# Kernel tuning notes

Hardware: AMD Instinct MI355X
Metric: run time of the kernel (lower is better)

The kernel has to match this reference:

```python
import jax, jax.numpy as jnp
import numpy as np

MODES = 16
WIDTH = 64
DEPTH = 4
MLP = 128


def spectral_conv(x, w_cplx):
    # x: [B, C, H, W] float32; w_cplx: [C, C, m1, m2] complex64
    B, C, H, W = x.shape
    x_ft = jnp.fft.rfft2(x)  # [B, C, H, W//2+1] complex
    m1, m2 = MODES, MODES
    low = jnp.einsum('bixy,ioxy->boxy', x_ft[:, :, :m1, :m2], w_cplx)
    out_ft = jnp.zeros((B, C, H, W // 2 + 1), dtype=jnp.complex64)
    out_ft = out_ft.at[:, :, :m1, :m2].set(low)
    return jnp.fft.irfft2(out_ft, s=(H, W)).astype(x.dtype)


def conv1x1(x, w, b):
    # x: [B,Cin,H,W], w: [Cout,Cin], b: [Cout]
    return jnp.einsum('bihw,oi->bohw', x, w) + b[None, :, None, None]


def setup_inputs() -> dict:
    key = jax.random.key(0)
    ks = jax.random.split(key, 4 + 4 * DEPTH)
    inp = {}
    inp['x'] = jax.random.normal(ks[0], (8, 3, 256, 256), dtype=jnp.float32)
    inp['fc0_w'] = jax.random.normal(ks[1], (WIDTH, 3), dtype=jnp.float32) * 0.1
    inp['fc0_b'] = jnp.zeros((WIDTH,), dtype=jnp.float32)
    scale = 1.0 / (WIDTH * WIDTH)
    sw_re, sw_im, ww, wb = [], [], [], []
    for i in range(DEPTH):
        k1, k2, k3 = jax.random.split(ks[4 + i], 3)
        sw_re.append(scale * jax.random.uniform(k1, (WIDTH, WIDTH, MODES, MODES), dtype=jnp.float32))
        sw_im.append(scale * jax.random.uniform(k2, (WIDTH, WIDTH, MODES, MODES), dtype=jnp.float32))
        ww.append(jax.random.normal(k3, (WIDTH, WIDTH), dtype=jnp.float32) * 0.05)
        wb.append(jnp.zeros((WIDTH,), dtype=jnp.float32))
    inp['spec_w_re'] = jnp.stack(sw_re)  # [D, C, C, m1, m2]
    inp['spec_w_im'] = jnp.stack(sw_im)
    inp['w_w'] = jnp.stack(ww)           # [D, C, C]
    inp['w_b'] = jnp.stack(wb)           # [D, C]
    inp['fc1_w'] = jax.random.normal(ks[2], (MLP, WIDTH), dtype=jnp.float32) * 0.05
    inp['fc1_b'] = jnp.zeros((MLP,), dtype=jnp.float32)
    inp['fc2_w'] = jax.random.normal(ks[3], (3, MLP), dtype=jnp.float32) * 0.05
    inp['fc2_b'] = jnp.zeros((3,), dtype=jnp.float32)
    return inp


def reference(x, fc0_w, fc0_b, spec_w_re, spec_w_im, w_w, w_b, fc1_w, fc1_b, fc2_w, fc2_b):
    # Dropout is identity in eval mode.
    h = conv1x1(x, fc0_w, fc0_b)  # [B, WIDTH, H, W]
    for i in range(DEPTH):
        w_cplx = spec_w_re[i] + 1j * spec_w_im[i]
        x1 = spectral_conv(h, w_cplx)
        x2 = conv1x1(h, w_w[i], w_b[i])
        h = jax.nn.relu(x1 + x2)
    h = jnp.transpose(h, (0, 2, 3, 1))  # [B, H, W, WIDTH]
    h = jax.nn.relu(jnp.einsum('bhwc,mc->bhwm', h, fc1_w) + fc1_b)
    h = jnp.einsum('bhwm,om->bhwo', h, fc2_w) + fc2_b
    return jnp.transpose(h, (0, 3, 1, 2))  # [B, 3, H, W]
```

## Files before the change

kernel.cpp:

```cpp
#include <hip/hip_runtime.h>

#define Hd 256
#define Wd 256
#define HW 65536
#define C 64
#define B 8
#define M 16
#define NDEPTH 4
#define NMLP 128

typedef __attribute__((ext_vector_type(8))) __bf16 bf16x8;
typedef __attribute__((ext_vector_type(4))) float f32x4;

__device__ inline void split_pack8(const float* v, uint4& hq, uint4& lq) {
    unsigned hw[4], lw[4];
#pragma unroll
    for (int i = 0; i < 4; ++i) {
        float a = v[2 * i], bb = v[2 * i + 1];
        unsigned ua = __float_as_uint(a);
        unsigned ha = (ua + 0x7fffu + ((ua >> 16) & 1u)) & 0xffff0000u;
        float ra = a - __uint_as_float(ha);
        unsigned ural = __float_as_uint(ra);
        unsigned la = (ural + 0x7fffu + ((ural >> 16) & 1u)) >> 16;
        unsigned ub = __float_as_uint(bb);
        unsigned hb = (ub + 0x7fffu + ((ub >> 16) & 1u)) & 0xffff0000u;
        float rb = bb - __uint_as_float(hb);
        unsigned urbl = __float_as_uint(rb);
        unsigned lb = (urbl + 0x7fffu + ((urbl >> 16) & 1u)) >> 16;
        hw[i] = (ha >> 16) | (hb & 0xffff0000u);
        lw[i] = la | (lb << 16);
    }
    hq = make_uint4(hw[0], hw[1], hw[2], hw[3]);
    lq = make_uint4(lw[0], lw[1], lw[2], lw[3]);
}

__global__ void k_table(float2* __restrict__ tab) {
    int t = threadIdx.x;
    double a = (6.283185307179586476925286766559 / 256.0) * (double)t;
    tab[t] = make_float2((float)cos(a), (float)sin(a));
}

__global__ void k_prep0(const float2* __restrict__ tab, const float* __restrict__ fc1w,
                        const float* __restrict__ ww,
                        float* __restrict__ trig, float* __restrict__ trigFT,
                        float* __restrict__ w1T, float* __restrict__ wwT_all) {
    int blk = blockIdx.x, t = threadIdx.x;
    if (blk < 32) {
        int k = blk & 15;
        float2 e = tab[(k * t) & 255];
        trig[blk * 256 + t] = (blk < 16) ? e.x : e.y;
    } else if (blk < 64) {
        int f = (blk - 32) * 256 + t;
        int y = f >> 5, kk = f & 31;
        float2 e = tab[((kk & 15) * y) & 255];
        trigFT[f] = (kk < 16) ? e.x : -e.y;
    } else if (blk < 96) {
        int f = (blk - 64) * 256 + t;
        int i = f >> 7, m = f & 127;
        w1T[f] = fc1w[m * 64 + i];
    } else {
        int f = (blk - 96) * 256 + t;
        int d = f >> 12, r = f & 4095;
        int i = r >> 6, o = r & 63;
        wwT_all[f] = ww[d * 4096 + o * 64 + i];
    }
}

__global__ void k_prep_et(const float2* __restrict__ tab,
                          uint4* __restrict__ ETh, uint4* __restrict__ ETl) {
    int c = blockIdx.x * 256 + threadIdx.x;
    if (c >= 1024) return;
    int ph = c >> 7, kc = (c >> 5) & 3, m = c & 31;
    float v[8];
#pragma unroll
    for (int j = 0; j < 8; ++j) {
        int y = ph * 32 + kc * 8 + j;
        float2 e = tab[((m & 15) * y) & 255];
        v[j] = (m < 16) ? e.x : -e.y;
    }
    uint4 hq, lq;
    split_pack8(v, hq, lq);
    ETh[c] = hq; ETl[c] = lq;
}

__global__ void k_fc0(const float* __restrict__ x, const float* __restrict__ w,
                      const float* __restrict__ bias, float* __restrict__ h) {
    int p = blockIdx.x * 256 + threadIdx.x;
    int b = p >> 16, pix = p & 65535;
    float x0 = x[(b * 3 + 0) * HW + pix];
    float x1 = x[(b * 3 + 1) * HW + pix];
    float x2 = x[(b * 3 + 2) * HW + pix];
    for (int o = 0; o < C; ++o) {
        float v = bias[o];
        v = fmaf(w[o * 3 + 0], x0, v);
        v = fmaf(w[o * 3 + 1], x1, v);
        v = fmaf(w[o * 3 + 2], x2, v);
        h[(b * C + o) * HW + pix] = v;
    }
}

__global__ __launch_bounds__(256, 4)
void k_fwd_y(const float* __restrict__ h, const uint4* __restrict__ ETh,
             const uint4* __restrict__ ETl, float* __restrict__ T1F) {
    __shared__ uint4 sBh[512], sBl[512];
    int blk = blockIdx.x;
    int xh = blk & 1, bc = blk >> 1;
    int x0 = xh * 128;
    int t = threadIdx.x;
    int xs = t & 127, half = t >> 7;
    int w = t >> 6, l = t & 63;
    int lr = l & 15, lq = l >> 4;
    f32x4 acc[2][2];
#pragma unroll
    for (int u = 0; u < 2; ++u)
#pragma unroll
        for (int xt = 0; xt < 2; ++xt) {
            acc[u][xt][0] = 0.f; acc[u][xt][1] = 0.f;
            acc[u][xt][2] = 0.f; acc[u][xt][3] = 0.f;
        }
    for (int ph = 0; ph < 8; ++ph) {
        {
            const float* src = h + (size_t)bc * HW + (ph * 32 + half * 16) * 256 + x0 + xs;
            float v[16];
#pragma unroll
            for (int kk = 0; kk < 16; ++kk) v[kk] = src[kk * 256];
#pragma unroll
            for (int c2 = 0; c2 < 2; ++c2) {
                uint4 hq4, lq4;
                split_pack8(v + c2 * 8, hq4, lq4);
                int cell = (half * 2 + c2) * 128 + xs;
                sBh[cell] = hq4; sBl[cell] = lq4;
            }
        }
        __syncthreads();
        bf16x8 Ah[2], Al[2];
#pragma unroll
        for (int u = 0; u < 2; ++u) {
            int ci = ph * 128 + lq * 32 + u * 16 + lr;
            Ah[u] = __builtin_bit_cast(bf16x8, ETh[ci]);
            Al[u] = __builtin_bit_cast(bf16x8, ETl[ci]);
        }
#pragma unroll
        for (int xt = 0; xt < 2; ++xt) {
            bf16x8 Bh = __builtin_bit_cast(bf16x8, sBh[lq * 128 + w * 32 + xt * 16 + lr]);
            bf16x8 Bl = __builtin_bit_cast(bf16x8, sBl[lq * 128 + w * 32 + xt * 16 + lr]);
#pragma unroll
            for (int u = 0; u < 2; ++u) {
                acc[u][xt] = __builtin_amdgcn_mfma_f32_16x16x32_bf16(Ah[u], Bh, acc[u][xt], 0, 0, 0);
                acc[u][xt] = __builtin_amdgcn_mfma_f32_16x16x32_bf16(Ah[u], Bl, acc[u][xt], 0, 0, 0);
                acc[u][xt] = __builtin_amdgcn_mfma_f32_16x16x32_bf16(Al[u], Bh, acc[u][xt], 0, 0, 0);
            }
        }
        __syncthreads();
    }
#pragma unroll
    for (int u = 0; u < 2; ++u)
#pragma unroll
        for (int xt = 0; xt < 2; ++xt)
#pragma unroll
            for (int g = 0; g < 4; ++g)
                T1F[(size_t)bc * 8192 + (u * 16 + lq * 4 + g) * 256 + x0 + w * 32 + xt * 16 + lr] =
                    acc[u][xt][g];
}

__global__ __launch_bounds__(256, 2)
void k_fwd_x(const float* __restrict__ T1F, const float* __restrict__ trig,
             float2* __restrict__ X) {
    __shared__ float sT[32 * 260];
    __shared__ float sG[32 * 260];
    int bc = blockIdx.x, t = threadIdx.x;
#pragma unroll
    for (int p = 0; p < 8; ++p) {
        int f = t + p * 256;
        int row = f >> 6, seg = f & 63;
        ((float4*)(sT + row * 260))[seg] = *(const float4*)(T1F + (size_t)bc * 8192 + f * 4);
        ((float4*)(sG + row * 260))[seg] = *(const float4*)(trig + row * 256 + seg * 4);
    }
    __syncthreads();
    int ky = t >> 4, kx = t & 15;
    const float* Tr = sT + ky * 260;
    const float* Ti = sT + (16 + ky) * 260;
    const float* Cs = sG + kx * 260;
    const float* Sn = sG + (16 + kx) * 260;
    float xr0 = 0.f, xi0 = 0.f, xr1 = 0.f, xi1 = 0.f;
    for (int q = 0; q < 64; q += 2) {
        float4 tr = *(const float4*)(Tr + q * 4);
        float4 ti = *(const float4*)(Ti + q * 4);
        float4 cs = *(const float4*)(Cs + q * 4);
        float4 sn = *(const float4*)(Sn + q * 4);
        xr0 = fmaf(tr.x, cs.x, xr0); xr0 = fmaf(ti.x, sn.x, xr0);
        xi0 = fmaf(ti.x, cs.x, xi0); xi0 = fmaf(-tr.x, sn.x, xi0);
        xr0 = fmaf(tr.y, cs.y, xr0); xr0 = fmaf(ti.y, sn.y, xr0);
        xi0 = fmaf(ti.y, cs.y, xi0); xi0 = fmaf(-tr.y, sn.y, xi0);
        xr0 = fmaf(tr.z, cs.z, xr0); xr0 = fmaf(ti.z, sn.z, xr0);
        xi0 = fmaf(ti.z, cs.z, xi0); xi0 = fmaf(-tr.z, sn.z, xi0);
        xr0 = fmaf(tr.w, cs.w, xr0); xr0 = fmaf(ti.w, sn.w, xr0);
        xi0 = fmaf(ti.w, cs.w, xi0); xi0 = fmaf(-tr.w, sn.w, xi0);
        float4 tr1 = *(const float4*)(Tr + q * 4 + 4);
        float4 ti1 = *(const float4*)(Ti + q * 4 + 4);
        float4 cs1 = *(const float4*)(Cs + q * 4 + 4);
        float4 sn1 = *(const float4*)(Sn + q * 4 + 4);
        xr1 = fmaf(tr1.x, cs1.x, xr1); xr1 = fmaf(ti1.x, sn1.x, xr1);
        xi1 = fmaf(ti1.x, cs1.x, xi1); xi1 = fmaf(-tr1.x, sn1.x, xi1);
        xr1 = fmaf(tr1.y, cs1.y, xr1); xr1 = fmaf(ti1.y, sn1.y, xr1);
        xi1 = fmaf(ti1.y, cs1.y, xi1); xi1 = fmaf(-tr1.y, sn1.y, xi1);
        xr1 = fmaf(tr1.z, cs1.z, xr1); xr1 = fmaf(ti1.z, sn1.z, xr1);
        xi1 = fmaf(ti1.z, cs1.z, xi1); xi1 = fmaf(-tr1.z, sn1.z, xi1);
        xr1 = fmaf(tr1.w, cs1.w, xr1); xr1 = fmaf(ti1.w, sn1.w, xr1);
        xi1 = fmaf(ti1.w, cs1.w, xi1); xi1 = fmaf(-tr1.w, sn1.w, xi1);
    }
    X[bc * 256 + t] = make_float2(xr0 + xr1, xi0 + xi1);
}

__global__ __launch_bounds__(256, 2)
void k_mix(const float2* __restrict__ X, const float* __restrict__ wre,
           const float* __restrict__ wim, float2* __restrict__ Y) {
    int o = blockIdx.x >> 2;
    int bq = blockIdx.x & 3;
    int m = threadIdx.x;
    int b0 = bq * 2, b1 = bq * 2 + 1;
    float yr0 = 0.f, yi0 = 0.f, yr1 = 0.f, yi1 = 0.f;
    for (int i = 0; i < C; ++i) {
        float wr = wre[(i * C + o) * 256 + m];
        float wi = wim[(i * C + o) * 256 + m];
        float2 x0 = X[(b0 * C + i) * 256 + m];
        float2 x1 = X[(b1 * C + i) * 256 + m];
        yr0 = fmaf(x0.x, wr, fmaf(-x0.y, wi, yr0));
        yi0 = fmaf(x0.x, wi, fmaf(x0.y, wr, yi0));
        yr1 = fmaf(x1.x, wr, fmaf(-x1.y, wi, yr1));
        yi1 = fmaf(x1.x, wi, fmaf(x1.y, wr, yi1));
    }
    Y[(b0 * C + o) * 256 + m] = make_float2(yr0, yi0);
    Y[(b1 * C + o) * 256 + m] = make_float2(yr1, yi1);
}

__global__ __launch_bounds__(256, 2)
void k_invy(const float2* __restrict__ Y, const float2* __restrict__ tab,
            float* __restrict__ Gq) {
    __shared__ float2 st[256];
    int blk = blockIdx.x;
    int yt = blk & 15, pg = (blk >> 4) & 3, b = blk >> 6;
    int t = threadIdx.x;
    st[t] = tab[t];
    int o = t & 63, kx = pg * 4 + (t >> 6);
    __syncthreads();
    float sc = (kx == 0 ? 1.0f : 2.0f) * (1.0f / 65536.0f);
    float yr[16], yi[16];
    const float2* yp = Y + (size_t)(b * 64 + o) * 256 + kx;
#pragma unroll
    for (int ky = 0; ky < 16; ++ky) {
        float2 v = yp[ky * 16];
        yr[ky] = v.x * sc;
        yi[ky] = v.y * sc;
    }
    int y0 = yt * 16;
    for (int yy = 0; yy < 16; ++yy) {
        int y = y0 + yy;
        float re = 0.f, im = 0.f;
#pragma unroll
        for (int ky = 0; ky < 16; ++ky) {
            float2 e = st[(ky * y) & 255];
            re = fmaf(yr[ky], e.x, re);
            re = fmaf(-yi[ky], e.y, re);
            im = fmaf(yr[ky], e.y, im);
            im = fmaf(yi[ky], e.x, im);
        }
        float* gp = Gq + (size_t)(b * 256 + y) * 32 * 64 + o;
        gp[kx * 64] = re;
        gp[(16 + kx) * 64] = -im;
    }
}

__global__ __launch_bounds__(256, 4)
void k_final(float* __restrict__ h, const float* __restrict__ Gq,
             const float* __restrict__ wwT, const float* __restrict__ wb,
             const float* __restrict__ trig) {
    __shared__ uint4 sHh[512], sHl[512];
    __shared__ uint4 sWh[256], sWl[256];
    int blk = blockIdx.x;
    int xq = blk & 1, y = (blk >> 1) & 255, b = blk >> 9;
    int x0 = xq * 128;
    int t = threadIdx.x;
    int xs = t & 127, half = t >> 7;
    int os = t & 63, q = t >> 6;
    int w = t >> 6, l = t & 63;
    int lr = l & 15, lq = l >> 4;
    f32x4 acc[8];
    {
        int ob = w * 16 + lq * 4;
        f32x4 ini;
        ini[0] = wb[ob]; ini[1] = wb[ob + 1]; ini[2] = wb[ob + 2]; ini[3] = wb[ob + 3];
#pragma unroll
        for (int xt = 0; xt < 8; ++xt) acc[xt] = ini;
    }
    for (int ph = 0; ph < 3; ++ph) {
        {
            const float* src; size_t str;
            if (ph < 2) {
                src = h + (size_t)(b * 64 + ph * 32 + half * 16) * HW + y * 256 + x0 + xs;
                str = HW;
            } else {
                src = trig + (half * 16) * 256 + x0 + xs;
                str = 256;
            }
            float v[16];
#pragma unroll
            for (int kk = 0; kk < 16; ++kk) v[kk] = src[(size_t)kk * str];
#pragma unroll
            for (int c2 = 0; c2 < 2; ++c2) {
                uint4 hq4, lq4;
                split_pack8(v + c2 * 8, hq4, lq4);
                int cell = (half * 2 + c2) * 128 + xs;
                sHh[cell] = hq4; sHl[cell] = lq4;
            }
        }
        {
            const float* src = (ph < 2)
                ? (wwT + (ph * 32 + q * 8) * 64 + os)
                : (Gq + ((size_t)(b * 256 + y) * 32 + q * 8) * 64 + os);
            float v[8];
#pragma unroll
            for (int kk = 0; kk < 8; ++kk) v[kk] = src[kk * 64];
            uint4 hq4, lq4;
            split_pack8(v, hq4, lq4);
            int cell = q * 64 + os;
            sWh[cell] = hq4; sWl[cell] = lq4;
        }
        __syncthreads();
        bf16x8 Ah = __builtin_bit_cast(bf16x8, sWh[lq * 64 + w * 16 + lr]);
        bf16x8 Al = __builtin_bit_cast(bf16x8, sWl[lq * 64 + w * 16 + lr]);
#pragma unroll
        for (int xt = 0; xt < 8; ++xt) {
            bf16x8 Bh = __builtin_bit_cast(bf16x8, sHh[lq * 128 + xt * 16 + lr]);
            bf16x8 Bl = __builtin_bit_cast(bf16x8, sHl[lq * 128 + xt * 16 + lr]);
            acc[xt] = __builtin_amdgcn_mfma_f32_16x16x32_bf16(Ah, Bh, acc[xt], 0, 0, 0);
            acc[xt] = __builtin_amdgcn_mfma_f32_16x16x32_bf16(Ah, Bl, acc[xt], 0, 0, 0);
            acc[xt] = __builtin_amdgcn_mfma_f32_16x16x32_bf16(Al, Bh, acc[xt], 0, 0, 0);
        }
        __syncthreads();
    }
#pragma unroll
    for (int g = 0; g < 4; ++g) {
        int o = w * 16 + lq * 4 + g;
        float* dst = h + (size_t)(b * 64 + o) * HW + y * 256 + x0 + lr;
#pragma unroll
        for (int xt = 0; xt < 8; ++xt)
            dst[xt * 16] = fmaxf(acc[xt][g], 0.f);
    }
}

__global__ __launch_bounds__(256, 3)
void k_fc12(const float* __restrict__ h, const float* __restrict__ w1T,
            const float* __restrict__ b1, const float* __restrict__ w2,
            const float* __restrict__ b2, float* __restrict__ out) {
    __shared__ uint4 sHh[512], sHl[512];
    __shared__ uint4 sWh[512], sWl[512];
    int blk = blockIdx.x;
    int xq = blk & 1, y = (blk >> 1) & 255, b = blk >> 9;
    int x0 = xq * 128;
    int t = threadIdx.x;
    int xs = t & 127, half = t >> 7;
    int w = t >> 6, l = t & 63;
    int lr = l & 15, lq = l >> 4;
    int mb = w * 32;
    f32x4 acc[2][8];
#pragma unroll
    for (int u = 0; u < 2; ++u) {
        int m0 = mb + u * 16 + lq * 4;
        f32x4 ini;
        ini[0] = b1[m0]; ini[1] = b1[m0 + 1]; ini[2] = b1[m0 + 2]; ini[3] = b1[m0 + 3];
#pragma unroll
        for (int xt = 0; xt < 8; ++xt) acc[u][xt] = ini;
    }
    for (int ph = 0; ph < 2; ++ph) {
        {
            const float* src = h + (size_t)(b * 64 + ph * 32 + half * 16) * HW + y * 256 + x0 + xs;
            float v[16];
#pragma unroll
            for (int kk = 0; kk < 16; ++kk) v[kk] = src[(size_t)kk * HW];
#pragma unroll
            for (int c2 = 0; c2 < 2; ++c2) {
                uint4 hq4, lq4;
                split_pack8(v + c2 * 8, hq4, lq4);
                int cell = (half * 2 + c2) * 128 + xs;
                sHh[cell] = hq4; sHl[cell] = lq4;
            }
        }
        {
            const float* src = w1T + (ph * 32 + half * 16) * 128 + xs;
            float v[16];
#pragma unroll
            for (int kk = 0; kk < 16; ++kk) v[kk] = src[kk * 128];
#pragma unroll
            for (int c2 = 0; c2 < 2; ++c2) {
                uint4 hq4, lq4;
                split_pack8(v + c2 * 8, hq4, lq4);
                int cell = (half * 2 + c2) * 128 + xs;
                sWh[cell] = hq4; sWl[cell] = lq4;
            }
        }
        __syncthreads();
        bf16x8 Ah[2], Al[2];
#pragma unroll
        for (int u = 0; u < 2; ++u) {
            Ah[u] = __builtin_bit_cast(bf16x8, sWh[lq * 128 + mb + u * 16 + lr]);
            Al[u] = __builtin_bit_cast(bf16x8, sWl[lq * 128 + mb + u * 16 + lr]);
        }
#pragma unroll
        for (int xt = 0; xt < 8; ++xt) {
            bf16x8 Bh = __builtin_bit_cast(bf16x8, sHh[lq * 128 + xt * 16 + lr]);
            bf16x8 Bl = __builtin_bit_cast(bf16x8, sHl[lq * 128 + xt * 16 + lr]);
#pragma unroll
            for (int u = 0; u < 2; ++u) {
                acc[u][xt] = __builtin_amdgcn_mfma_f32_16x16x32_bf16(Ah[u], Bh, acc[u][xt], 0, 0, 0);
                acc[u][xt] = __builtin_amdgcn_mfma_f32_16x16x32_bf16(Ah[u], Bl, acc[u][xt], 0, 0, 0);
                acc[u][xt] = __builtin_amdgcn_mfma_f32_16x16x32_bf16(Al[u], Bh, acc[u][xt], 0, 0, 0);
            }
        }
        __syncthreads();
    }
    float pj[3][8];
#pragma unroll
    for (int j = 0; j < 3; ++j)
#pragma unroll
        for (int xt = 0; xt < 8; ++xt) pj[j][xt] = 0.f;
#pragma unroll
    for (int u = 0; u < 2; ++u)
#pragma unroll
        for (int g = 0; g < 4; ++g) {
            int m = mb + u * 16 + lq * 4 + g;
            float w20 = w2[m], w21 = w2[NMLP + m], w22 = w2[2 * NMLP + m];
#pragma unroll
            for (int xt = 0; xt < 8; ++xt) {
                float r = fmaxf(acc[u][xt][g], 0.f);
                pj[0][xt] = fmaf(w20, r, pj[0][xt]);
                pj[1][xt] = fmaf(w21, r, pj[1][xt]);
                pj[2][xt] = fmaf(w22, r, pj[2][xt]);
            }
        }
#pragma unroll
    for (int j = 0; j < 3; ++j)
#pragma unroll
        for (int xt = 0; xt < 8; ++xt) {
            float v = pj[j][xt];
            v += __shfl_xor(v, 16);
            v += __shfl_xor(v, 32);
            pj[j][xt] = v;
        }
    float* part = (float*)sHh;
    if (lq == 0) {
#pragma unroll
        for (int j = 0; j < 3; ++j)
#pragma unroll
            for (int xt = 0; xt < 8; ++xt)
                part[(w * 3 + j) * 128 + xt * 16 + lr] = pj[j][xt];
    }
    __syncthreads();
#pragma unroll
    for (int r = 0; r < 2; ++r) {
        int idx = t + r * 256;
        if (idx < 384) {
            int j = idx >> 7, xx = idx & 127;
            float s = b2[j];
#pragma unroll
            for (int ww2 = 0; ww2 < 4; ++ww2) s += part[(ww2 * 3 + j) * 128 + xx];
            out[(size_t)(b * 3 + j) * HW + y * 256 + x0 + xx] = s;
        }
    }
}

extern "C" void kernel_launch(void* const* d_in, const int* in_sizes, int n_in,
                              void* d_out, int out_size, void* d_ws, size_t ws_size,
                              hipStream_t stream) {
    const float* x     = (const float*)d_in[0];
    const float* fc0_w = (const float*)d_in[1];
    const float* fc0_b = (const float*)d_in[2];
    const float* swre  = (const float*)d_in[3];
    const float* swim  = (const float*)d_in[4];
    const float* ww    = (const float*)d_in[5];
    const float* wb    = (const float*)d_in[6];
    const float* fc1w  = (const float*)d_in[7];
    const float* fc1b  = (const float*)d_in[8];
    const float* fc2w  = (const float*)d_in[9];
    const float* fc2b  = (const float*)d_in[10];

    float* ws = (float*)d_ws;
    float2* tab    = (float2*)ws;
    float*  h      = ws + 512;
    float*  T1F    = ws + 33554944;
    float2* X      = (float2*)(ws + 37749248);
    float2* Y      = (float2*)(ws + 38011392);
    float*  Gq     = ws + 38273536;
    float*  wwT    = ws + 42467840;
    float*  w1T    = ws + 42484224;
    float*  trig   = ws + 42492416;
    float*  trigFT = ws + 42500608;
    uint4*  ETh    = (uint4*)(ws + 42508800);
    uint4*  ETl    = (uint4*)(ws + 42512896);

    k_table<<<dim3(1), dim3(256), 0, stream>>>(tab);
    k_prep0<<<dim3(160), dim3(256), 0, stream>>>(tab, fc1w, ww, trig, trigFT, w1T, wwT);
    k_prep_et<<<dim3(4), dim3(256), 0, stream>>>(tab, ETh, ETl);
    k_fc0<<<dim3(2048), dim3(256), 0, stream>>>(x, fc0_w, fc0_b, h);

    for (int d = 0; d < NDEPTH; ++d) {
        k_fwd_y<<<dim3(1024), dim3(256), 0, stream>>>(h, ETh, ETl, T1F);
        k_fwd_x<<<dim3(512), dim3(256), 0, stream>>>(T1F, trig, X);
        k_mix<<<dim3(256), dim3(256), 0, stream>>>(X, swre + (size_t)d * C * C * 256,
                                                   swim + (size_t)d * C * C * 256, Y);
        k_invy<<<dim3(512), dim3(256), 0, stream>>>(Y, tab, Gq);
        k_final<<<dim3(4096), dim3(256), 0, stream>>>(h, Gq, wwT + d * 4096, wb + d * C, trig);
    }
    k_fc12<<<dim3(4096), dim3(256), 0, stream>>>(h, w1T, fc1b, fc2w, fc2b, (float*)d_out);
}
```

Before: 630.5 us.

## Register double-buffer global loads and use lgkm-only barriers in GEMM kernels

```diff
diff --git a/kernel.cpp b/kernel.cpp
--- a/kernel.cpp
+++ b/kernel.cpp
@@ -11,6 +11,11 @@
 
 typedef __attribute__((ext_vector_type(8))) __bf16 bf16x8;
 typedef __attribute__((ext_vector_type(4))) float f32x4;
+
+__device__ inline void bar_lgkm() {
+    asm volatile("s_waitcnt lgkmcnt(0)" ::: "memory");
+    __builtin_amdgcn_s_barrier();
+}
 
 __device__ inline void split_pack8(const float* v, uint4& hq, uint4& lq) {
     unsigned hw[4], lw[4];
@@ -118,21 +123,30 @@
             acc[u][xt][0] = 0.f; acc[u][xt][1] = 0.f;
             acc[u][xt][2] = 0.f; acc[u][xt][3] = 0.f;
         }
+    const float* hb = h + (size_t)bc * HW + (half * 16) * 256 + x0 + xs;
+    float v0[16], v1[16];
+    auto loadv = [&](float* vv, int ph) {
+        const float* src = hb + ph * 32 * 256;
+#pragma unroll
+        for (int kk = 0; kk < 16; ++kk) vv[kk] = src[kk * 256];
+    };
+    auto stage = [&](const float* vv) {
+#pragma unroll
+        for (int c2 = 0; c2 < 2; ++c2) {
+            uint4 hq4, lq4;
+            split_pack8(vv + c2 * 8, hq4, lq4);
+            int cell = (half * 2 + c2) * 128 + xs;
+            sBh[cell] = hq4; sBl[cell] = lq4;
+        }
+    };
+    loadv(v0, 0);
+#pragma unroll
     for (int ph = 0; ph < 8; ++ph) {
-        {
-            const float* src = h + (size_t)bc * HW + (ph * 32 + half * 16) * 256 + x0 + xs;
-            float v[16];
-#pragma unroll
-            for (int kk = 0; kk < 16; ++kk) v[kk] = src[kk * 256];
-#pragma unroll
-            for (int c2 = 0; c2 < 2; ++c2) {
-                uint4 hq4, lq4;
-                split_pack8(v + c2 * 8, hq4, lq4);
-                int cell = (half * 2 + c2) * 128 + xs;
-                sBh[cell] = hq4; sBl[cell] = lq4;
-            }
-        }
-        __syncthreads();
+        const float* cur = (ph & 1) ? v1 : v0;
+        float* nxt = (ph & 1) ? v0 : v1;
+        if (ph < 7) loadv(nxt, ph + 1);
+        stage(cur);
+        bar_lgkm();
         bf16x8 Ah[2], Al[2];
 #pragma unroll
         for (int u = 0; u < 2; ++u) {
@@ -151,7 +165,7 @@
                 acc[u][xt] = __builtin_amdgcn_mfma_f32_16x16x32_bf16(Al[u], Bh, acc[u][xt], 0, 0, 0);
             }
         }
-        __syncthreads();
+        bar_lgkm();
     }
 #pragma unroll
     for (int u = 0; u < 2; ++u)
@@ -293,40 +307,48 @@
 #pragma unroll
         for (int xt = 0; xt < 8; ++xt) acc[xt] = ini;
     }
+    float vh0[16], vh1[16], vw0[8], vw1[8];
+    auto loadH = [&](float* vv, int ph) {
+        const float* src; size_t str;
+        if (ph < 2) {
+            src = h + (size_t)(b * 64 + ph * 32 + half * 16) * HW + y * 256 + x0 + xs;
+            str = HW;
+        } else {
+            src = trig + (half * 16) * 256 + x0 + xs;
+            str = 256;
+        }
+#pragma unroll
+        for (int kk = 0; kk < 16; ++kk) vv[kk] = src[(size_t)kk * str];
+    };
+    auto loadW = [&](float* vv, int ph) {
+        const float* src = (ph < 2)
+            ? (wwT + (ph * 32 + q * 8) * 64 + os)
+            : (Gq + ((size_t)(b * 256 + y) * 32 + q * 8) * 64 + os);
+#pragma unroll
+        for (int kk = 0; kk < 8; ++kk) vv[kk] = src[kk * 64];
+    };
+    loadH(vh0, 0); loadW(vw0, 0);
+#pragma unroll
     for (int ph = 0; ph < 3; ++ph) {
+        const float* cH = (ph & 1) ? vh1 : vh0;
+        float* nH = (ph & 1) ? vh0 : vh1;
+        const float* cW = (ph & 1) ? vw1 : vw0;
+        float* nW = (ph & 1) ? vw0 : vw1;
+        if (ph < 2) { loadH(nH, ph + 1); loadW(nW, ph + 1); }
+#pragma unroll
+        for (int c2 = 0; c2 < 2; ++c2) {
+            uint4 hq4, lq4;
+            split_pack8(cH + c2 * 8, hq4, lq4);
+            int cell = (half * 2 + c2) * 128 + xs;
+            sHh[cell] = hq4; sHl[cell] = lq4;
+        }
         {
-            const float* src; size_t str;
-            if (ph < 2) {
-                src = h + (size_t)(b * 64 + ph * 32 + half * 16) * HW + y * 256 + x0 + xs;
-                str = HW;
-            } else {
-                src = trig + (half * 16) * 256 + x0 + xs;
-                str = 256;
-            }
-            float v[16];
-#pragma unroll
-            for (int kk = 0; kk < 16; ++kk) v[kk] = src[(size_t)kk * str];
-#pragma unroll
-            for (int c2 = 0; c2 < 2; ++c2) {
-                uint4 hq4, lq4;
-                split_pack8(v + c2 * 8, hq4, lq4);
-                int cell = (half * 2 + c2) * 128 + xs;
-                sHh[cell] = hq4; sHl[cell] = lq4;
-            }
-        }
-        {
-            const float* src = (ph < 2)
-                ? (wwT + (ph * 32 + q * 8) * 64 + os)
-                : (Gq + ((size_t)(b * 256 + y) * 32 + q * 8) * 64 + os);
-            float v[8];
-#pragma unroll
-            for (int kk = 0; kk < 8; ++kk) v[kk] = src[kk * 64];
             uint4 hq4, lq4;
-            split_pack8(v, hq4, lq4);
+            split_pack8(cW, hq4, lq4);
             int cell = q * 64 + os;
             sWh[cell] = hq4; sWl[cell] = lq4;
         }
-        __syncthreads();
+        bar_lgkm();
         bf16x8 Ah = __builtin_bit_cast(bf16x8, sWh[lq * 64 + w * 16 + lr]);
         bf16x8 Al = __builtin_bit_cast(bf16x8, sWl[lq * 64 + w * 16 + lr]);
 #pragma unroll
@@ -337,7 +359,7 @@
             acc[xt] = __builtin_amdgcn_mfma_f32_16x16x32_bf16(Ah, Bl, acc[xt], 0, 0, 0);
             acc[xt] = __builtin_amdgcn_mfma_f32_16x16x32_bf16(Al, Bh, acc[xt], 0, 0, 0);
         }
-        __syncthreads();
+        bar_lgkm();
     }
 #pragma unroll
     for (int g = 0; g < 4; ++g) {
@@ -349,7 +371,7 @@
     }
 }
 
-__global__ __launch_bounds__(256, 3)
+__global__ __launch_bounds__(256, 4)
 void k_fc12(const float* __restrict__ h, const float* __restrict__ w1T,
             const float* __restrict__ b1, const float* __restrict__ w2,
             const float* __restrict__ b2, float* __restrict__ out) {
@@ -372,19 +394,24 @@
 #pragma unroll
         for (int xt = 0; xt < 8; ++xt) acc[u][xt] = ini;
     }
+    float vh0[16], vh1[16];
+    auto loadH = [&](float* vv, int ph) {
+        const float* src = h + (size_t)(b * 64 + ph * 32 + half * 16) * HW + y * 256 + x0 + xs;
+#pragma unroll
+        for (int kk = 0; kk < 16; ++kk) vv[kk] = src[(size_t)kk * HW];
+    };
+    loadH(vh0, 0);
+#pragma unroll
     for (int ph = 0; ph < 2; ++ph) {
-        {
-            const float* src = h + (size_t)(b * 64 + ph * 32 + half * 16) * HW + y * 256 + x0 + xs;
-            float v[16];
-#pragma unroll
-            for (int kk = 0; kk < 16; ++kk) v[kk] = src[(size_t)kk * HW];
-#pragma unroll
-            for (int c2 = 0; c2 < 2; ++c2) {
-                uint4 hq4, lq4;
-                split_pack8(v + c2 * 8, hq4, lq4);
-                int cell = (half * 2 + c2) * 128 + xs;
-                sHh[cell] = hq4; sHl[cell] = lq4;
-            }
+        const float* cH = (ph & 1) ? vh1 : vh0;
+        float* nH = (ph & 1) ? vh0 : vh1;
+        if (ph < 1) loadH(nH, ph + 1);
+#pragma unroll
+        for (int c2 = 0; c2 < 2; ++c2) {
+            uint4 hq4, lq4;
+            split_pack8(cH + c2 * 8, hq4, lq4);
+            int cell = (half * 2 + c2) * 128 + xs;
+            sHh[cell] = hq4; sHl[cell] = lq4;
         }
         {
             const float* src = w1T + (ph * 32 + half * 16) * 128 + xs;
@@ -399,7 +426,7 @@
                 sWh[cell] = hq4; sWl[cell] = lq4;
             }
         }
-        __syncthreads();
+        bar_lgkm();
         bf16x8 Ah[2], Al[2];
 #pragma unroll
         for (int u = 0; u < 2; ++u) {
@@ -417,7 +444,7 @@
                 acc[u][xt] = __builtin_amdgcn_mfma_f32_16x16x32_bf16(Al[u], Bh, acc[u][xt], 0, 0, 0);
             }
         }
-        __syncthreads();
+        bar_lgkm();
     }
     float pj[3][8];
 #pragma unroll
```

Measured after the change: 618.5 us. Within noise of the previous version (-1.9%).

## Store activations as pre-split bf16 hi/lo in MFMA-ready channel-packed layout

Applied to the files above, without the earlier changes.

```diff
diff --git a/kernel.cpp b/kernel.cpp
--- a/kernel.cpp
+++ b/kernel.cpp
@@ -11,6 +11,11 @@
 
 typedef __attribute__((ext_vector_type(8))) __bf16 bf16x8;
 typedef __attribute__((ext_vector_type(4))) float f32x4;
+
+__device__ inline void bar_lgkm() {
+    asm volatile("s_waitcnt lgkmcnt(0)" ::: "memory");
+    __builtin_amdgcn_s_barrier();
+}
 
 __device__ inline void split_pack8(const float* v, uint4& hq, uint4& lq) {
     unsigned hw[4], lw[4];
@@ -34,6 +39,29 @@
     lq = make_uint4(lw[0], lw[1], lw[2], lw[3]);
 }
 
+__device__ inline void split_pack4(const float* v, uint2& hq, uint2& lq) {
+    unsigned hw[2], lw[2];
+#pragma unroll
+    for (int i = 0; i < 2; ++i) {
+        float a = v[2 * i], bb = v[2 * i + 1];
+        unsigned ua = __float_as_uint(a);
+        unsigned ha = (ua + 0x7fffu + ((ua >> 16) & 1u)) & 0xffff0000u;
+        float ra = a - __uint_as_float(ha);
+        unsigned ural = __float_as_uint(ra);
+        unsigned la = (ural + 0x7fffu + ((ural >> 16) & 1u)) >> 16;
+        unsigned ub = __float_as_uint(bb);
+        unsigned hb = (ub + 0x7fffu + ((ub >> 16) & 1u)) & 0xffff0000u;
+        float rb = bb - __uint_as_float(hb);
+        unsigned urbl = __float_as_uint(rb);
+        unsigned lb = (urbl + 0x7fffu + ((urbl >> 16) & 1u)) >> 16;
+        hw[i] = (ha >> 16) | (hb & 0xffff0000u);
+        lw[i] = la | (lb << 16);
+    }
+    hq = make_uint2(hw[0], hw[1]);
+    lq = make_uint2(lw[0], lw[1]);
+}
+
+
 __global__ void k_table(float2* __restrict__ tab) {
     int t = threadIdx.x;
     double a = (6.283185307179586476925286766559 / 256.0) * (double)t;
@@ -41,28 +69,45 @@
 }
 
 __global__ void k_prep0(const float2* __restrict__ tab, const float* __restrict__ fc1w,
-                        const float* __restrict__ ww,
-                        float* __restrict__ trig, float* __restrict__ trigFT,
-                        float* __restrict__ w1T, float* __restrict__ wwT_all) {
+                        const float* __restrict__ ww, float* __restrict__ trig,
+                        uint4* __restrict__ trigs_h, uint4* __restrict__ trigs_l,
+                        uint4* __restrict__ wws_h, uint4* __restrict__ wws_l,
+                        uint4* __restrict__ w1s_h, uint4* __restrict__ w1s_l) {
     int blk = blockIdx.x, t = threadIdx.x;
     if (blk < 32) {
         int k = blk & 15;
         float2 e = tab[(k * t) & 255];
         trig[blk * 256 + t] = (blk < 16) ? e.x : e.y;
-    } else if (blk < 64) {
-        int f = (blk - 32) * 256 + t;
-        int y = f >> 5, kk = f & 31;
-        float2 e = tab[((kk & 15) * y) & 255];
-        trigFT[f] = (kk < 16) ? e.x : -e.y;
-    } else if (blk < 96) {
-        int f = (blk - 64) * 256 + t;
-        int i = f >> 7, m = f & 127;
-        w1T[f] = fc1w[m * 64 + i];
+    } else if (blk < 36) {
+        int idx = (blk - 32) * 256 + t;
+        int kc = idx >> 8, x = idx & 255;
+        float v[8];
+#pragma unroll
+        for (int j = 0; j < 8; ++j) {
+            int row = kc * 8 + j;
+            float2 e = tab[((row & 15) * x) & 255];
+            v[j] = (row < 16) ? e.x : e.y;
+        }
+        uint4 hq, lq; split_pack8(v, hq, lq);
+        trigs_h[idx] = hq; trigs_l[idx] = lq;
+    } else if (blk < 44) {
+        int idx = (blk - 36) * 256 + t;
+        int o = idx & 63, kc = (idx >> 6) & 3, ph = (idx >> 8) & 1, d = idx >> 9;
+        float v[8];
+#pragma unroll
+        for (int j = 0; j < 8; ++j)
+            v[j] = ww[d * 4096 + o * 64 + ph * 32 + kc * 8 + j];
+        uint4 hq, lq; split_pack8(v, hq, lq);
+        wws_h[idx] = hq; wws_l[idx] = lq;
     } else {
-        int f = (blk - 96) * 256 + t;
-        int d = f >> 12, r = f & 4095;
-        int i = r >> 6, o = r & 63;
-        wwT_all[f] = ww[d * 4096 + o * 64 + i];
+        int idx = (blk - 44) * 256 + t;
+        int m = idx & 127, kc = (idx >> 7) & 3, ph = idx >> 9;
+        float v[8];
+#pragma unroll
+        for (int j = 0; j < 8; ++j)
+            v[j] = fc1w[m * 64 + ph * 32 + kc * 8 + j];
+        uint4 hq, lq; split_pack8(v, hq, lq);
+        w1s_h[idx] = hq; w1s_l[idx] = lq;
     }
 }
 
@@ -84,27 +129,43 @@
 }
 
 __global__ void k_fc0(const float* __restrict__ x, const float* __restrict__ w,
-                      const float* __restrict__ bias, float* __restrict__ h) {
+                      const float* __restrict__ bias,
+                      uint4* __restrict__ hs_h, uint4* __restrict__ hs_l) {
     int p = blockIdx.x * 256 + threadIdx.x;
     int b = p >> 16, pix = p & 65535;
+    int y = pix >> 8, xx = pix & 255;
     float x0 = x[(b * 3 + 0) * HW + pix];
     float x1 = x[(b * 3 + 1) * HW + pix];
     float x2 = x[(b * 3 + 2) * HW + pix];
-    for (int o = 0; o < C; ++o) {
-        float v = bias[o];
-        v = fmaf(w[o * 3 + 0], x0, v);
-        v = fmaf(w[o * 3 + 1], x1, v);
-        v = fmaf(w[o * 3 + 2], x2, v);
-        h[(b * C + o) * HW + pix] = v;
+    size_t rb = (size_t)(b * 256 + y) * 8;
+#pragma unroll
+    for (int cc = 0; cc < 8; ++cc) {
+        float v[8];
+#pragma unroll
+        for (int j = 0; j < 8; ++j) {
+            int o = cc * 8 + j;
+            float s = bias[o];
+            s = fmaf(w[o * 3 + 0], x0, s);
+            s = fmaf(w[o * 3 + 1], x1, s);
+            s = fmaf(w[o * 3 + 2], x2, s);
+            v[j] = s;
+        }
+        uint4 hq, lq; split_pack8(v, hq, lq);
+        size_t cell = (rb + cc) * 256 + xx;
+        hs_h[cell] = hq; hs_l[cell] = lq;
     }
 }
 
 __global__ __launch_bounds__(256, 4)
-void k_fwd_y(const float* __restrict__ h, const uint4* __restrict__ ETh,
-             const uint4* __restrict__ ETl, float* __restrict__ T1F) {
+void k_fwd_y(const uint4* __restrict__ hs_h, const uint4* __restrict__ hs_l,
+             const uint4* __restrict__ ETh, const uint4* __restrict__ ETl,
+             float* __restrict__ T1F) {
     __shared__ uint4 sBh[512], sBl[512];
     int blk = blockIdx.x;
-    int xh = blk & 1, bc = blk >> 1;
+    int rest = blk & 127, cl = blk >> 7;
+    int cc = rest & 7, xh = (rest >> 3) & 1, b = rest >> 4;
+    int c = cc * 8 + cl;
+    int bc = b * 64 + c;
     int x0 = xh * 128;
     int t = threadIdx.x;
     int xs = t & 127, half = t >> 7;
@@ -118,21 +179,45 @@
             acc[u][xt][0] = 0.f; acc[u][xt][1] = 0.f;
             acc[u][xt][2] = 0.f; acc[u][xt][3] = 0.f;
         }
+    const ushort* ph16 = (const ushort*)hs_h;
+    const ushort* pl16 = (const ushort*)hs_l;
+    size_t cbase = ((size_t)(b * 256) * 8 + cc) * 256 + x0 + xs;
+    unsigned hv0[16], lv0[16], hv1[16], lv1[16];
+    auto loadv = [&](unsigned* hv, unsigned* lv, int ph) {
+        size_t a = (cbase + (size_t)(ph * 32 + half * 16) * 2048) * 8 + cl;
+#pragma unroll
+        for (int kk = 0; kk < 16; ++kk) {
+            hv[kk] = ph16[a + kk * 16384];
+            lv[kk] = pl16[a + kk * 16384];
+        }
+    };
+    auto stage = [&](const unsigned* hv, const unsigned* lv) {
+#pragma unroll
+        for (int c2 = 0; c2 < 2; ++c2) {
+            int o8 = c2 * 8;
+            uint4 hq, lqq;
+            hq.x = hv[o8 + 0] | (hv[o8 + 1] << 16);
+            hq.y = hv[o8 + 2] | (hv[o8 + 3] << 16);
+            hq.z = hv[o8 + 4] | (hv[o8 + 5] << 16);
+            hq.w = hv[o8 + 6] | (hv[o8 + 7] << 16);
+            lqq.x = lv[o8 + 0] | (lv[o8 + 1] << 16);
+            lqq.y = lv[o8 + 2] | (lv[o8 + 3] << 16);
+            lqq.z = lv[o8 + 4] | (lv[o8 + 5] << 16);
+            lqq.w = lv[o8 + 6] | (lv[o8 + 7] << 16);
+            int cell = (half * 2 + c2) * 128 + xs;
+            sBh[cell] = hq; sBl[cell] = lqq;
+        }
+    };
+    loadv(hv0, lv0, 0);
+#pragma unroll
     for (int ph = 0; ph < 8; ++ph) {
-        {
-            const float* src = h + (size_t)bc * HW + (ph * 32 + half * 16) * 256 + x0 + xs;
-            float v[16];
-#pragma unroll
-            for (int kk = 0; kk < 16; ++kk) v[kk] = src[kk * 256];
-#pragma unroll
-            for (int c2 = 0; c2 < 2; ++c2) {
-                uint4 hq4, lq4;
-                split_pack8(v + c2 * 8, hq4, lq4);
-                int cell = (half * 2 + c2) * 128 + xs;
-                sBh[cell] = hq4; sBl[cell] = lq4;
-            }
-        }
-        __syncthreads();
+        const unsigned* chv = (ph & 1) ? hv1 : hv0;
+        const unsigned* clv = (ph & 1) ? lv1 : lv0;
+        unsigned* nhv = (ph & 1) ? hv0 : hv1;
+        unsigned* nlv = (ph & 1) ? lv0 : lv1;
+        if (ph < 7) loadv(nhv, nlv, ph + 1);
+        stage(chv, clv);
+        bar_lgkm();
         bf16x8 Ah[2], Al[2];
 #pragma unroll
         for (int u = 0; u < 2; ++u) {
@@ -151,7 +236,7 @@
                 acc[u][xt] = __builtin_amdgcn_mfma_f32_16x16x32_bf16(Al[u], Bh, acc[u][xt], 0, 0, 0);
             }
         }
-        __syncthreads();
+        bar_lgkm();
     }
 #pragma unroll
     for (int u = 0; u < 2; ++u)
@@ -272,19 +357,22 @@
 }
 
 __global__ __launch_bounds__(256, 4)
-void k_final(float* __restrict__ h, const float* __restrict__ Gq,
-             const float* __restrict__ wwT, const float* __restrict__ wb,
-             const float* __restrict__ trig) {
-    __shared__ uint4 sHh[512], sHl[512];
-    __shared__ uint4 sWh[256], sWl[256];
+void k_final(uint4* __restrict__ hs_h, uint4* __restrict__ hs_l,
+             const float* __restrict__ Gq,
+             const uint4* __restrict__ wws_h, const uint4* __restrict__ wws_l,
+             const float* __restrict__ wb,
+             const uint4* __restrict__ trigs_h, const uint4* __restrict__ trigs_l) {
+    __shared__ uint4 sH0h[512], sH0l[512], sH1h[512], sH1l[512];
+    __shared__ uint4 sGh[256], sGl[256];
     int blk = blockIdx.x;
     int xq = blk & 1, y = (blk >> 1) & 255, b = blk >> 9;
     int x0 = xq * 128;
     int t = threadIdx.x;
-    int xs = t & 127, half = t >> 7;
     int os = t & 63, q = t >> 6;
     int w = t >> 6, l = t & 63;
     int lr = l & 15, lq = l >> 4;
+    int kc0 = t >> 7, xsa = t & 127;
+    size_t hbase = (size_t)(b * 256 + y) * 8;
     f32x4 acc[8];
     {
         int ob = w * 16 + lq * 4;
@@ -293,76 +381,97 @@
 #pragma unroll
         for (int xt = 0; xt < 8; ++xt) acc[xt] = ini;
     }
-    for (int ph = 0; ph < 3; ++ph) {
-        {
-            const float* src; size_t str;
-            if (ph < 2) {
-                src = h + (size_t)(b * 64 + ph * 32 + half * 16) * HW + y * 256 + x0 + xs;
-                str = HW;
-            } else {
-                src = trig + (half * 16) * 256 + x0 + xs;
-                str = 256;
-            }
-            float v[16];
-#pragma unroll
-            for (int kk = 0; kk < 16; ++kk) v[kk] = src[(size_t)kk * str];
-#pragma unroll
-            for (int c2 = 0; c2 < 2; ++c2) {
-                uint4 hq4, lq4;
-                split_pack8(v + c2 * 8, hq4, lq4);
-                int cell = (half * 2 + c2) * 128 + xs;
-                sHh[cell] = hq4; sHl[cell] = lq4;
-            }
-        }
-        {
-            const float* src = (ph < 2)
-                ? (wwT + (ph * 32 + q * 8) * 64 + os)
-                : (Gq + ((size_t)(b * 256 + y) * 32 + q * 8) * 64 + os);
-            float v[8];
-#pragma unroll
-            for (int kk = 0; kk < 8; ++kk) v[kk] = src[kk * 64];
-            uint4 hq4, lq4;
-            split_pack8(v, hq4, lq4);
-            int cell = q * 64 + os;
-            sWh[cell] = hq4; sWl[cell] = lq4;
-        }
-        __syncthreads();
-        bf16x8 Ah = __builtin_bit_cast(bf16x8, sWh[lq * 64 + w * 16 + lr]);
-        bf16x8 Al = __builtin_bit_cast(bf16x8, sWl[lq * 64 + w * 16 + lr]);
+    float gv[8];
+    {
+        const float* gsrc = Gq + ((size_t)(b * 256 + y) * 32 + q * 8) * 64 + os;
+#pragma unroll
+        for (int kk = 0; kk < 8; ++kk) gv[kk] = gsrc[kk * 64];
+    }
+    uint4 A0h = wws_h[lq * 64 + w * 16 + lr];
+    uint4 A0l = wws_l[lq * 64 + w * 16 + lr];
+    uint4 A1h = wws_h[(4 + lq) * 64 + w * 16 + lr];
+    uint4 A1l = wws_l[(4 + lq) * 64 + w * 16 + lr];
+    uint4 h0a = hs_h[(hbase + kc0) * 256 + x0 + xsa];
+    uint4 l0a = hs_l[(hbase + kc0) * 256 + x0 + xsa];
+    uint4 h0b = hs_h[(hbase + 2 + kc0) * 256 + x0 + xsa];
+    uint4 l0b = hs_l[(hbase + 2 + kc0) * 256 + x0 + xsa];
+    uint4 h1a = hs_h[(hbase + 4 + kc0) * 256 + x0 + xsa];
+    uint4 l1a = hs_l[(hbase + 4 + kc0) * 256 + x0 + xsa];
+    uint4 h1b = hs_h[(hbase + 6 + kc0) * 256 + x0 + xsa];
+    uint4 l1b = hs_l[(hbase + 6 + kc0) * 256 + x0 + xsa];
+    {
+        uint4 ghq, glq; split_pack8(gv, ghq, glq);
+        sGh[q * 64 + os] = ghq; sGl[q * 64 + os] = glq;
+    }
+    sH0h[t] = h0a; sH0h[t + 256] = h0b;
+    sH0l[t] = l0a; sH0l[t + 256] = l0b;
+    bar_lgkm();
+    sH1h[t] = h1a; sH1h[t + 256] = h1b;
+    sH1l[t] = l1a; sH1l[t + 256] = l1b;
+#pragma unroll
+    for (int xt = 0; xt < 8; ++xt) {
+        bf16x8 Bh = __builtin_bit_cast(bf16x8, sH0h[lq * 128 + xt * 16 + lr]);
+        bf16x8 Bl = __builtin_bit_cast(bf16x8, sH0l[lq * 128 + xt * 16 + lr]);
+        bf16x8 Ah = __builtin_bit_cast(bf16x8, A0h);
+        bf16x8 Al = __builtin_bit_cast(bf16x8, A0l);
+        acc[xt] = __builtin_amdgcn_mfma_f32_16x16x32_bf16(Ah, Bh, acc[xt], 0, 0, 0);
+        acc[xt] = __builtin_amdgcn_mfma_f32_16x16x32_bf16(Ah, Bl, acc[xt], 0, 0, 0);
+        acc[xt] = __builtin_amdgcn_mfma_f32_16x16x32_bf16(Al, Bh, acc[xt], 0, 0, 0);
+    }
+    bar_lgkm();
+#pragma unroll
+    for (int xt = 0; xt < 8; ++xt) {
+        bf16x8 Bh = __builtin_bit_cast(bf16x8, sH1h[lq * 128 + xt * 16 + lr]);
+        bf16x8 Bl = __builtin_bit_cast(bf16x8, sH1l[lq * 128 + xt * 16 + lr]);
+        bf16x8 Ah = __builtin_bit_cast(bf16x8, A1h);
+        bf16x8 Al = __builtin_bit_cast(bf16x8, A1l);
+        acc[xt] = __builtin_amdgcn_mfma_f32_16x16x32_bf16(Ah, Bh, acc[xt], 0, 0, 0);
+        acc[xt] = __builtin_amdgcn_mfma_f32_16x16x32_bf16(Ah, Bl, acc[xt], 0, 0, 0);
+        acc[xt] = __builtin_amdgcn_mfma_f32_16x16x32_bf16(Al, Bh, acc[xt], 0, 0, 0);
+    }
+    {
+        bf16x8 Ah = __builtin_bit_cast(bf16x8, sGh[lq * 64 + w * 16 + lr]);
+        bf16x8 Al = __builtin_bit_cast(bf16x8, sGl[lq * 64 + w * 16 + lr]);
 #pragma unroll
         for (int xt = 0; xt < 8; ++xt) {
-            bf16x8 Bh = __builtin_bit_cast(bf16x8, sHh[lq * 128 + xt * 16 + lr]);
-            bf16x8 Bl = __builtin_bit_cast(bf16x8, sHl[lq * 128 + xt * 16 + lr]);
+            bf16x8 Bh = __builtin_bit_cast(bf16x8, trigs_h[lq * 256 + x0 + xt * 16 + lr]);
+            bf16x8 Bl = __builtin_bit_cast(bf16x8, trigs_l[lq * 256 + x0 + xt * 16 + lr]);
             acc[xt] = __builtin_amdgcn_mfma_f32_16x16x32_bf16(Ah, Bh, acc[xt], 0, 0, 0);
             acc[xt] = __builtin_amdgcn_mfma_f32_16x16x32_bf16(Ah, Bl, acc[xt], 0, 0, 0);
             acc[xt] = __builtin_amdgcn_mfma_f32_16x16x32_bf16(Al, Bh, acc[xt], 0, 0, 0);
         }
-        __syncthreads();
-    }
-#pragma unroll
-    for (int g = 0; g < 4; ++g) {
-        int o = w * 16 + lq * 4 + g;
-        float* dst = h + (size_t)(b * 64 + o) * HW + y * 256 + x0 + lr;
-#pragma unroll
-        for (int xt = 0; xt < 8; ++xt)
-            dst[xt * 16] = fmaxf(acc[xt][g], 0.f);
+    }
+    uint2* hp_h = (uint2*)hs_h;
+    uint2* hp_l = (uint2*)hs_l;
+    int ccw = w * 2 + (lq >> 1);
+    int halfsel = lq & 1;
+#pragma unroll
+    for (int xt = 0; xt < 8; ++xt) {
+        float r[4];
+#pragma unroll
+        for (int g = 0; g < 4; ++g) r[g] = fmaxf(acc[xt][g], 0.f);
+        uint2 hq, lqd; split_pack4(r, hq, lqd);
+        size_t gc = (hbase + ccw) * 256 + x0 + xt * 16 + lr;
+        hp_h[gc * 2 + halfsel] = hq;
+        hp_l[gc * 2 + halfsel] = lqd;
     }
 }
 
 __global__ __launch_bounds__(256, 3)
-void k_fc12(const float* __restrict__ h, const float* __restrict__ w1T,
+void k_fc12(const uint4* __restrict__ hs_h, const uint4* __restrict__ hs_l,
+            const uint4* __restrict__ w1s_h, const uint4* __restrict__ w1s_l,
             const float* __restrict__ b1, const float* __restrict__ w2,
             const float* __restrict__ b2, float* __restrict__ out) {
-    __shared__ uint4 sHh[512], sHl[512];
-    __shared__ uint4 sWh[512], sWl[512];
+    __shared__ uint4 sH0h[512], sH0l[512], sH1h[512], sH1l[512];
     int blk = blockIdx.x;
     int xq = blk & 1, y = (blk >> 1) & 255, b = blk >> 9;
     int x0 = xq * 128;
     int t = threadIdx.x;
-    int xs = t & 127, half = t >> 7;
     int w = t >> 6, l = t & 63;
     int lr = l & 15, lq = l >> 4;
     int mb = w * 32;
+    int kc0 = t >> 7, xsa = t & 127;
+    size_t hbase = (size_t)(b * 256 + y) * 8;
     f32x4 acc[2][8];
 #pragma unroll
     for (int u = 0; u < 2; ++u) {
@@ -372,52 +481,53 @@
 #pragma unroll
         for (int xt = 0; xt < 8; ++xt) acc[u][xt] = ini;
     }
-    for (int ph = 0; ph < 2; ++ph) {
-        {
-            const float* src = h + (size_t)(b * 64 + ph * 32 + half * 16) * HW + y * 256 + x0 + xs;
-            float v[16];
-#pragma unroll
-            for (int kk = 0; kk < 16; ++kk) v[kk] = src[(size_t)kk * HW];
-#pragma unroll
-            for (int c2 = 0; c2 < 2; ++c2) {
-                uint4 hq4, lq4;
-                split_pack8(v + c2 * 8, hq4, lq4);
-                int cell = (half * 2 + c2) * 128 + xs;
-                sHh[cell] = hq4; sHl[cell] = lq4;
-            }
-        }
-        {
-            const float* src = w1T + (ph * 32 + half * 16) * 128 + xs;
-            float v[16];
-#pragma unroll
-            for (int kk = 0; kk < 16; ++kk) v[kk] = src[kk * 128];
-#pragma unroll
-            for (int c2 = 0; c2 < 2; ++c2) {
-                uint4 hq4, lq4;
-                split_pack8(v + c2 * 8, hq4, lq4);
-                int cell = (half * 2 + c2) * 128 + xs;
-                sWh[cell] = hq4; sWl[cell] = lq4;
-            }
-        }
-        __syncthreads();
-        bf16x8 Ah[2], Al[2];
+    uint4 a0h[2], a0l[2], a1h[2], a1l[2];
+#pragma unroll
+    for (int u = 0; u < 2; ++u) {
+        a0h[u] = w1s_h[lq * 128 + mb + u * 16 + lr];
+        a0l[u] = w1s_l[lq * 128 + mb + u * 16 + lr];
+        a1h[u] = w1s_h[(4 + lq) * 128 + mb + u * 16 + lr];
+        a1l[u] = w1s_l[(4 + lq) * 128 + mb + u * 16 + lr];
+    }
+    uint4 h0a = hs_h[(hbase + kc0) * 256 + x0 + xsa];
+    uint4 l0a = hs_l[(hbase + kc0) * 256 + x0 + xsa];
+    uint4 h0b = hs_h[(hbase + 2 + kc0) * 256 + x0 + xsa];
+    uint4 l0b = hs_l[(hbase + 2 + kc0) * 256 + x0 + xsa];
+    uint4 h1a = hs_h[(hbase + 4 + kc0) * 256 + x0 + xsa];
+    uint4 l1a = hs_l[(hbase + 4 + kc0) * 256 + x0 + xsa];
+    uint4 h1b = hs_h[(hbase + 6 + kc0) * 256 + x0 + xsa];
+    uint4 l1b = hs_l[(hbase + 6 + kc0) * 256 + x0 + xsa];
+    sH0h[t] = h0a; sH0h[t + 256] = h0b;
+    sH0l[t] = l0a; sH0l[t + 256] = l0b;
+    bar_lgkm();
+    sH1h[t] = h1a; sH1h[t + 256] = h1b;
+    sH1l[t] = l1a; sH1l[t + 256] = l1b;
+#pragma unroll
+    for (int xt = 0; xt < 8; ++xt) {
+        bf16x8 Bh = __builtin_bit_cast(bf16x8, sH0h[lq * 128 + xt * 16 + lr]);
+        bf16x8 Bl = __builtin_bit_cast(bf16x8, sH0l[lq * 128 + xt * 16 + lr]);
 #pragma unroll
         for (int u = 0; u < 2; ++u) {
-            Ah[u] = __builtin_bit_cast(bf16x8, sWh[lq * 128 + mb + u * 16 + lr]);
-            Al[u] = __builtin_bit_cast(bf16x8, sWl[lq * 128 + mb + u * 16 + lr]);
-        }
-#pragma unroll
-        for (int xt = 0; xt < 8; ++xt) {
-            bf16x8 Bh = __builtin_bit_cast(bf16x8, sHh[lq * 128 + xt * 16 + lr]);
-            bf16x8 Bl = __builtin_bit_cast(bf16x8, sHl[lq * 128 + xt * 16 + lr]);
-#pragma unroll
-            for (int u = 0; u < 2; ++u) {
-                acc[u][xt] = __builtin_amdgcn_mfma_f32_16x16x32_bf16(Ah[u], Bh, acc[u][xt], 0, 0, 0);
-                acc[u][xt] = __builtin_amdgcn_mfma_f32_16x16x32_bf16(Ah[u], Bl, acc[u][xt], 0, 0, 0);
-                acc[u][xt] = __builtin_amdgcn_mfma_f32_16x16x32_bf16(Al[u], Bh, acc[u][xt], 0, 0, 0);
-            }
-        }
-        __syncthreads();
+            bf16x8 Ah = __builtin_bit_cast(bf16x8, a0h[u]);
+            bf16x8 Al = __builtin_bit_cast(bf16x8, a0l[u]);
+            acc[u][xt] = __builtin_amdgcn_mfma_f32_16x16x32_bf16(Ah, Bh, acc[u][xt], 0, 0, 0);
+            acc[u][xt] = __builtin_amdgcn_mfma_f32_16x16x32_bf16(Ah, Bl, acc[u][xt], 0, 0, 0);
+            acc[u][xt] = __builtin_amdgcn_mfma_f32_16x16x32_bf16(Al, Bh, acc[u][xt], 0, 0, 0);
+        }
+    }
+    bar_lgkm();
+#pragma unroll
+    for (int xt = 0; xt < 8; ++xt) {
+        bf16x8 Bh = __builtin_bit_cast(bf16x8, sH1h[lq * 128 + xt * 16 + lr]);
+        bf16x8 Bl = __builtin_bit_cast(bf16x8, sH1l[lq * 128 + xt * 16 + lr]);
+#pragma unroll
+        for (int u = 0; u < 2; ++u) {
+            bf16x8 Ah = __builtin_bit_cast(bf16x8, a1h[u]);
+            bf16x8 Al = __builtin_bit_cast(bf16x8, a1l[u]);
+            acc[u][xt] = __builtin_amdgcn_mfma_f32_16x16x32_bf16(Ah, Bh, acc[u][xt], 0, 0, 0);
+            acc[u][xt] = __builtin_amdgcn_mfma_f32_16x16x32_bf16(Ah, Bl, acc[u][xt], 0, 0, 0);
+            acc[u][xt] = __builtin_amdgcn_mfma_f32_16x16x32_bf16(Al, Bh, acc[u][xt], 0, 0, 0);
+        }
     }
     float pj[3][8];
 #pragma unroll
@@ -447,7 +557,7 @@
             v += __shfl_xor(v, 32);
             pj[j][xt] = v;
         }
-    float* part = (float*)sHh;
+    float* part = (float*)sH0h;
     if (lq == 0) {
 #pragma unroll
         for (int j = 0; j < 3; ++j)
@@ -485,31 +595,41 @@
     const float* fc2b  = (const float*)d_in[10];
 
     float* ws = (float*)d_ws;
-    float2* tab    = (float2*)ws;
-    float*  h      = ws + 512;
-    float*  T1F    = ws + 33554944;
-    float2* X      = (float2*)(ws + 37749248);
-    float2* Y      = (float2*)(ws + 38011392);
-    float*  Gq     = ws + 38273536;
-    float*  wwT    = ws + 42467840;
-    float*  w1T    = ws + 42484224;
-    float*  trig   = ws + 42492416;
-    float*  trigFT = ws + 42500608;
-    uint4*  ETh    = (uint4*)(ws + 42508800);
-    uint4*  ETl    = (uint4*)(ws + 42512896);
+    float2* tab     = (float2*)ws;
+    uint4*  hs_h    = (uint4*)(ws + 512);
+    uint4*  hs_l    = (uint4*)(ws + 512 + 16777216);
+    float*  T1F     = ws + 33554944;
+    float2* X       = (float2*)(ws + 37749248);
+    float2* Y       = (float2*)(ws + 38011392);
+    float*  Gq      = ws + 38273536;
+    float*  trig    = ws + 42467840;
+    uint4*  trigs_h = (uint4*)(ws + 42476032);
+    uint4*  trigs_l = (uint4*)(ws + 42480128);
+    uint4*  wws_h   = (uint4*)(ws + 42484224);
+    uint4*  wws_l   = (uint4*)(ws + 42492416);
+    uint4*  w1s_h   = (uint4*)(ws + 42500608);
+    uint4*  w1s_l   = (uint4*)(ws + 42504704);
+    uint4*  ETh     = (uint4*)(ws + 42508800);
+    uint4*  ETl     = (uint4*)(ws + 42512896);
 
     k_table<<<dim3(1), dim3(256), 0, stream>>>(tab);
-    k_prep0<<<dim3(160), dim3(256), 0, stream>>>(tab, fc1w, ww, trig, trigFT, w1T, wwT);
+    k_prep0<<<dim3(48), dim3(256), 0, stream>>>(tab, fc1w, ww, trig,
+                                                trigs_h, trigs_l, wws_h, wws_l,
+                                                w1s_h, w1s_l);
     k_prep_et<<<dim3(4), dim3(256), 0, stream>>>(tab, ETh, ETl);
-    k_fc0<<<dim3(2048), dim3(256), 0, stream>>>(x, fc0_w, fc0_b, h);
+    k_fc0<<<dim3(2048), dim3(256), 0, stream>>>(x, fc0_w, fc0_b, hs_h, hs_l);
 
     for (int d = 0; d < NDEPTH; ++d) {
-        k_fwd_y<<<dim3(1024), dim3(256), 0, stream>>>(h, ETh, ETl, T1F);
+        k_fwd_y<<<dim3(1024), dim3(256), 0, stream>>>(hs_h, hs_l, ETh, ETl, T1F);
         k_fwd_x<<<dim3(512), dim3(256), 0, stream>>>(T1F, trig, X);
         k_mix<<<dim3(256), dim3(256), 0, stream>>>(X, swre + (size_t)d * C * C * 256,
                                                    swim + (size_t)d * C * C * 256, Y);
         k_invy<<<dim3(512), dim3(256), 0, stream>>>(Y, tab, Gq);
-        k_final<<<dim3(4096), dim3(256), 0, stream>>>(h, Gq, wwT + d * 4096, wb + d * C, trig);
-    }
-    k_fc12<<<dim3(4096), dim3(256), 0, stream>>>(h, w1T, fc1b, fc2w, fc2b, (float*)d_out);
-}
+        k_final<<<dim3(4096), dim3(256), 0, stream>>>(hs_h, hs_l, Gq,
+                                                      wws_h + (size_t)d * 512,
+                                                      wws_l + (size_t)d * 512,
+                                                      wb + d * C, trigs_h, trigs_l);
+    }
+    k_fc12<<<dim3(4096), dim3(256), 0, stream>>>(hs_h, hs_l, w1s_h, w1s_l,
+                                                 fc1b, fc2w, fc2b, (float*)d_out);
+}
```

New measurement: 878.8 us. 1.39x slower.
